# Kernel optimization log

Hardware: AMD Instinct MI355X
Metric: run time of the kernel (lower is better)

The kernel has to match this reference:

```python
import jax, jax.numpy as jnp
import numpy as np

D_MODEL = 256
NUM_UNIVERSES = 8
D_UNIVERSE = D_MODEL // NUM_UNIVERSES
B, S = 1, 1024
TEMP = 5.0
NEG = -1e9


def setup_inputs() -> dict:
    key = jax.random.key(0)
    ks = jax.random.split(key, 5)
    scale = 1.0 / np.sqrt(D_MODEL)
    return {
        "x": jax.random.normal(ks[0], (B, S, D_MODEL), dtype=jnp.float32),
        "Wq": jax.random.normal(ks[1], (D_MODEL, D_MODEL), dtype=jnp.float32) * scale,
        "bq": jnp.zeros((D_MODEL,), dtype=jnp.float32),
        "Wk": jax.random.normal(ks[2], (D_MODEL, D_MODEL), dtype=jnp.float32) * scale,
        "bk": jnp.zeros((D_MODEL,), dtype=jnp.float32),
        "Wv": jax.random.normal(ks[3], (D_MODEL, D_MODEL), dtype=jnp.float32) * scale,
        "bv": jnp.zeros((D_MODEL,), dtype=jnp.float32),
        "Wo": jax.random.normal(ks[4], (D_MODEL, D_MODEL), dtype=jnp.float32) * scale,
        "bo": jnp.zeros((D_MODEL,), dtype=jnp.float32),
    }


def reference(x, Wq, bq, Wk, bk, Wv, bv, Wo, bo):
    b, s, d = x.shape
    h, du = NUM_UNIVERSES, D_UNIVERSE
    # Projections; Q,K squashed to [0,1] fuzzy truth values
    Q = jax.nn.sigmoid(x @ Wq + bq)
    K = jax.nn.sigmoid(x @ Wk + bk)
    V = x @ Wv + bv
    # [B,S,D] -> [B,H,S,du]
    Q = Q.reshape(b, s, h, du).transpose(0, 2, 1, 3)
    K = K.reshape(b, s, h, du).transpose(0, 2, 1, 3)
    V = V.reshape(b, s, h, du).transpose(0, 2, 1, 3)
    # Fuzzy implication: clamp(1 - Q_i + K_j, max=1), mean over d_universe
    # Broadcast to [B,H,S,S,du] (the memory-heavy intermediate)
    implication = jnp.minimum(1.0 - Q[:, :, :, None, :] + K[:, :, None, :, :], 1.0)
    truth = implication.mean(axis=-1)  # [B,H,S,S]
    # Causal mask
    causal = jnp.tril(jnp.ones((s, s), dtype=bool))
    truth = jnp.where(causal[None, None], truth, NEG)
    attn = jax.nn.softmax(truth * TEMP, axis=-1)
    out = jnp.einsum("bhij,bhjd->bhid", attn, V)
    out = out.transpose(0, 2, 1, 3).reshape(b, s, d)
    return out @ Wo + bo
```

## Files before the change

### kernel.cpp

```cpp
#include <hip/hip_runtime.h>
#include <math.h>

#define S_LEN 1024
#define DM    256
#define DU    32
#define TEMPF 5.0f
#define NS    4

__global__ __launch_bounds__(256) void qkv_proj_kernel(
    const float* __restrict__ x,
    const float* __restrict__ Wq, const float* __restrict__ bq,
    const float* __restrict__ Wk, const float* __restrict__ bk,
    const float* __restrict__ Wv, const float* __restrict__ bv,
    float* __restrict__ qo, float* __restrict__ ko, float* __restrict__ vo)
{
    const int mat = blockIdx.z;
    const float* __restrict__ W    = (mat == 0) ? Wq : ((mat == 1) ? Wk : Wv);
    const float* __restrict__ bias = (mat == 0) ? bq : ((mat == 1) ? bk : bv);
    float* __restrict__ dst        = (mat == 0) ? qo : ((mat == 1) ? ko : vo);

    const int n0 = blockIdx.x * 64;
    const int m0 = blockIdx.y * 32;
    const int t  = threadIdx.x;
    const int tx = t & 15;
    const int ty = t >> 4;

    __shared__ float xs[2][32][36];
    __shared__ float wsh[2][32][68];

    float acc[2][4] = {};

    const int xrow = t & 31;
    const int xkc  = (t >> 5) * 4;
    const int wrow = t >> 4;
    const int wcol = (t & 15) * 4;

    float4 xa = *(const float4*)&x[(m0 + xrow) * DM + xkc];
    float4 wa = *(const float4*)&W[wrow * DM + n0 + wcol];
    float4 wb = *(const float4*)&W[(wrow + 16) * DM + n0 + wcol];
    xs[0][xkc + 0][xrow] = xa.x; xs[0][xkc + 1][xrow] = xa.y;
    xs[0][xkc + 2][xrow] = xa.z; xs[0][xkc + 3][xrow] = xa.w;
    *(float4*)&wsh[0][wrow][wcol]      = wa;
    *(float4*)&wsh[0][wrow + 16][wcol] = wb;
    __syncthreads();

    int cur = 0;
    for (int k0 = 32; k0 < DM; k0 += 32) {
        xa = *(const float4*)&x[(m0 + xrow) * DM + k0 + xkc];
        wa = *(const float4*)&W[(k0 + wrow) * DM + n0 + wcol];
        wb = *(const float4*)&W[(k0 + wrow + 16) * DM + n0 + wcol];
        #pragma unroll
        for (int kk = 0; kk < 32; kk++) {
            float2 a2 = *(const float2*)&xs[cur][kk][ty * 2];
            float4 b4 = *(const float4*)&wsh[cur][kk][tx * 4];
            acc[0][0] += a2.x * b4.x; acc[0][1] += a2.x * b4.y;
            acc[0][2] += a2.x * b4.z; acc[0][3] += a2.x * b4.w;
            acc[1][0] += a2.y * b4.x; acc[1][1] += a2.y * b4.y;
            acc[1][2] += a2.y * b4.z; acc[1][3] += a2.y * b4.w;
        }
        const int nxt = cur ^ 1;
        xs[nxt][xkc + 0][xrow] = xa.x; xs[nxt][xkc + 1][xrow] = xa.y;
        xs[nxt][xkc + 2][xrow] = xa.z; xs[nxt][xkc + 3][xrow] = xa.w;
        *(float4*)&wsh[nxt][wrow][wcol]      = wa;
        *(float4*)&wsh[nxt][wrow + 16][wcol] = wb;
        __syncthreads();
        cur = nxt;
    }
    #pragma unroll
    for (int kk = 0; kk < 32; kk++) {
        float2 a2 = *(const float2*)&xs[cur][kk][ty * 2];
        float4 b4 = *(const float4*)&wsh[cur][kk][tx * 4];
        acc[0][0] += a2.x * b4.x; acc[0][1] += a2.x * b4.y;
        acc[0][2] += a2.x * b4.z; acc[0][3] += a2.x * b4.w;
        acc[1][0] += a2.y * b4.x; acc[1][1] += a2.y * b4.y;
        acc[1][2] += a2.y * b4.z; acc[1][3] += a2.y * b4.w;
    }

    #pragma unroll
    for (int j = 0; j < 4; j++) {
        const int cidx = n0 + tx * 4 + j;
        const float bb = bias[cidx];
        const int hh = cidx >> 5;
        const int dd = cidx & 31;
        #pragma unroll
        for (int i = 0; i < 2; i++) {
            const int row = m0 + ty * 2 + i;
            float val = acc[i][j] + bb;
            if (mat < 2) val = 1.0f / (1.0f + __expf(-val));
            dst[hh * (S_LEN * DU) + row * DU + dd] = val;
        }
    }
}

__global__ __launch_bounds__(256) void attn_kernel(
    const float* __restrict__ q, const float* __restrict__ k,
    const float* __restrict__ v,
    float* __restrict__ part_o, float* __restrict__ part_ml)
{
    const int bid = blockIdx.x;
    const int it2 = 31 - (bid >> 5);
    const int sub = bid & 31;
    const int h   = sub & 7;
    const int s   = sub >> 3;
    const int t   = threadIdx.x;
    const int r   = t >> 4;
    const int c   = t & 15;
    const int ig0 = it2 * 32 + r;
    const int ig1 = ig0 + 16;

    __shared__ float  Ks[64][36];
    __shared__ float2 Vs2[64][17];
    __shared__ float  Ps[32][68];

    float qreg0[32], qreg1[32];
    {
        const float* q0 = q + h * (S_LEN * DU) + ig0 * DU;
        const float* q1 = q + h * (S_LEN * DU) + ig1 * DU;
        #pragma unroll
        for (int d4 = 0; d4 < 8; d4++) {
            float4 a = *(const float4*)&q0[d4 * 4];
            float4 b = *(const float4*)&q1[d4 * 4];
            qreg0[d4 * 4 + 0] = a.x; qreg0[d4 * 4 + 1] = a.y;
            qreg0[d4 * 4 + 2] = a.z; qreg0[d4 * 4 + 3] = a.w;
            qreg1[d4 * 4 + 0] = b.x; qreg1[d4 * 4 + 1] = b.y;
            qreg1[d4 * 4 + 2] = b.z; qreg1[d4 * 4 + 3] = b.w;
        }
    }

    float m0r = -1e30f, m1r = -1e30f, l0 = 0.0f, l1 = 0.0f;
    float o00 = 0.0f, o01 = 0.0f, o10 = 0.0f, o11 = 0.0f;

    const int njt = it2 / 2 + 1;
    for (int jt = s; jt < njt; jt += NS) {
        __syncthreads();
        {
            const int jr  = t >> 2;
            const int d0k = (t & 3) * 8;
            const int dv  = (t & 3) * 4;
            const float* kp = k + h * (S_LEN * DU) + (jt * 64 + jr) * DU;
            const float* vp = v + h * (S_LEN * DU) + (jt * 64 + jr) * DU;
            float4 ka = *(const float4*)&kp[d0k];
            float4 kb = *(const float4*)&kp[d0k + 4];
            float4 va4 = *(const float4*)&vp[dv];
            float4 vb4 = *(const float4*)&vp[dv + 16];
            *(float4*)&Ks[jr][d0k]     = ka;
            *(float4*)&Ks[jr][d0k + 4] = kb;
            Vs2[jr][dv + 0] = make_float2(va4.x, vb4.x);
            Vs2[jr][dv + 1] = make_float2(va4.y, vb4.y);
            Vs2[jr][dv + 2] = make_float2(va4.z, vb4.z);
            Vs2[jr][dv + 3] = make_float2(va4.w, vb4.w);
        }
        __syncthreads();

        float zv0[4], zv1[4];
        #pragma unroll
        for (int q4 = 0; q4 < 4; q4++) {
            const int jj  = c + q4 * 16;
            const int jgl = jt * 64 + jj;
            float s0 = 0.0f, s1 = 0.0f;
            #pragma unroll
            for (int d = 0; d < 32; d += 4) {
                float4 k4 = *(const float4*)&Ks[jj][d];
                s0 += fmaxf(qreg0[d + 0] - k4.x, 0.0f)
                    + fmaxf(qreg0[d + 1] - k4.y, 0.0f)
                    + fmaxf(qreg0[d + 2] - k4.z, 0.0f)
                    + fmaxf(qreg0[d + 3] - k4.w, 0.0f);
                s1 += fmaxf(qreg1[d + 0] - k4.x, 0.0f)
                    + fmaxf(qreg1[d + 1] - k4.y, 0.0f)
                    + fmaxf(qreg1[d + 2] - k4.z, 0.0f)
                    + fmaxf(qreg1[d + 3] - k4.w, 0.0f);
            }
            zv0[q4] = (jgl <= ig0) ? (TEMPF - (TEMPF / 32.0f) * s0) : -1e30f;
            zv1[q4] = (jgl <= ig1) ? (TEMPF - (TEMPF / 32.0f) * s1) : -1e30f;
        }

        float mloc0 = fmaxf(fmaxf(zv0[0], zv0[1]), fmaxf(zv0[2], zv0[3]));
        float mloc1 = fmaxf(fmaxf(zv1[0], zv1[1]), fmaxf(zv1[2], zv1[3]));
        #pragma unroll
        for (int off = 8; off; off >>= 1) {
            mloc0 = fmaxf(mloc0, __shfl_xor(mloc0, off, 16));
            mloc1 = fmaxf(mloc1, __shfl_xor(mloc1, off, 16));
        }
        const float mn0 = fmaxf(m0r, mloc0), mn1 = fmaxf(m1r, mloc1);
        const float al0 = __expf(m0r - mn0), al1 = __expf(m1r - mn1);

        float ll0 = 0.0f, ll1 = 0.0f;
        #pragma unroll
        for (int q4 = 0; q4 < 4; q4++) {
            const float p0 = __expf(zv0[q4] - mn0);
            const float p1 = __expf(zv1[q4] - mn1);
            ll0 += p0; ll1 += p1;
            Ps[r][c + q4 * 16]      = p0;
            Ps[r + 16][c + q4 * 16] = p1;
        }
        #pragma unroll
        for (int off = 8; off; off >>= 1) {
            ll0 += __shfl_xor(ll0, off, 16);
            ll1 += __shfl_xor(ll1, off, 16);
        }

        float pv00 = 0.0f, pv01 = 0.0f, pv10 = 0.0f, pv11 = 0.0f;
        #pragma unroll 4
        for (int j4 = 0; j4 < 64; j4 += 4) {
            float4 pj0 = *(const float4*)&Ps[r][j4];
            float4 pj1 = *(const float4*)&Ps[r + 16][j4];
            float2 va = Vs2[j4 + 0][c];
            float2 vb = Vs2[j4 + 1][c];
            float2 vc2 = Vs2[j4 + 2][c];
            float2 vd = Vs2[j4 + 3][c];
            pv00 += pj0.x * va.x + pj0.y * vb.x + pj0.z * vc2.x + pj0.w * vd.x;
            pv01 += pj0.x * va.y + pj0.y * vb.y + pj0.z * vc2.y + pj0.w * vd.y;
            pv10 += pj1.x * va.x + pj1.y * vb.x + pj1.z * vc2.x + pj1.w * vd.x;
            pv11 += pj1.x * va.y + pj1.y * vb.y + pj1.z * vc2.y + pj1.w * vd.y;
        }

        m0r = mn0; l0 = l0 * al0 + ll0; o00 = o00 * al0 + pv00; o01 = o01 * al0 + pv01;
        m1r = mn1; l1 = l1 * al1 + ll1; o10 = o10 * al1 + pv10; o11 = o11 * al1 + pv11;
    }

    const int pbase = (h * 32 + it2) * NS + s;
    float* po = part_o + pbase * 1024;
    po[r * 32 + c]             = o00;
    po[r * 32 + c + 16]        = o01;
    po[(r + 16) * 32 + c]      = o10;
    po[(r + 16) * 32 + c + 16] = o11;
    if (c == 0) {
        *(float2*)&part_ml[pbase * 64 + r * 2]        = make_float2(m0r, l0);
        *(float2*)&part_ml[pbase * 64 + (r + 16) * 2] = make_float2(m1r, l1);
    }
}

__global__ __launch_bounds__(256) void combine_kernel(
    const float* __restrict__ part_o, const float* __restrict__ part_ml,
    float* __restrict__ attn)
{
    const int h   = blockIdx.x & 7;
    const int it2 = blockIdx.x >> 3;
    const int t   = threadIdx.x;
    const int r   = t >> 4;
    const int c   = t & 15;
    const int base = (h * 32 + it2) * NS;

    float2 ml0[NS], ml1[NS];
    #pragma unroll
    for (int s2 = 0; s2 < NS; s2++) {
        ml0[s2] = *(const float2*)&part_ml[(base + s2) * 64 + r * 2];
        ml1[s2] = *(const float2*)&part_ml[(base + s2) * 64 + (r + 16) * 2];
    }
    float M0 = ml0[0].x, M1 = ml1[0].x;
    #pragma unroll
    for (int s2 = 1; s2 < NS; s2++) {
        M0 = fmaxf(M0, ml0[s2].x);
        M1 = fmaxf(M1, ml1[s2].x);
    }
    float L0 = 0.0f, L1 = 0.0f, a00 = 0.0f, a01 = 0.0f, a10 = 0.0f, a11 = 0.0f;
    #pragma unroll
    for (int s2 = 0; s2 < NS; s2++) {
        const float w0 = __expf(ml0[s2].x - M0);
        const float w1 = __expf(ml1[s2].x - M1);
        L0 += w0 * ml0[s2].y;
        L1 += w1 * ml1[s2].y;
        const float* po = part_o + (base + s2) * 1024;
        a00 += w0 * po[r * 32 + c];
        a01 += w0 * po[r * 32 + c + 16];
        a10 += w1 * po[(r + 16) * 32 + c];
        a11 += w1 * po[(r + 16) * 32 + c + 16];
    }
    const float i0 = 1.0f / L0, i1 = 1.0f / L1;
    attn[(it2 * 32 + r) * DM + h * DU + c]           = a00 * i0;
    attn[(it2 * 32 + r) * DM + h * DU + c + 16]      = a01 * i0;
    attn[(it2 * 32 + r + 16) * DM + h * DU + c]      = a10 * i1;
    attn[(it2 * 32 + r + 16) * DM + h * DU + c + 16] = a11 * i1;
}

__global__ __launch_bounds__(256) void out_proj_kernel(
    const float* __restrict__ a, const float* __restrict__ W,
    const float* __restrict__ bias, float* __restrict__ dst)
{
    const int n0 = blockIdx.x * 32;
    const int m0 = blockIdx.y * 32;
    const int t  = threadIdx.x;
    const int tx = t & 15;
    const int ty = t >> 4;

    __shared__ float xs[2][32][36];
    __shared__ float wsh[2][32][36];

    float acc[2][2] = {};

    const int arow = t & 31;
    const int akc  = (t >> 5) * 4;
    const int wr   = t >> 3;
    const int wc   = (t & 7) * 4;

    float4 xa = *(const float4*)&a[(m0 + arow) * DM + akc];
    float4 wa = *(const float4*)&W[wr * DM + n0 + wc];
    xs[0][akc + 0][arow] = xa.x; xs[0][akc + 1][arow] = xa.y;
    xs[0][akc + 2][arow] = xa.z; xs[0][akc + 3][arow] = xa.w;
    *(float4*)&wsh[0][wr][wc] = wa;
    __syncthreads();

    int cur = 0;
    for (int k0 = 32; k0 < DM; k0 += 32) {
        xa = *(const float4*)&a[(m0 + arow) * DM + k0 + akc];
        wa = *(const float4*)&W[(k0 + wr) * DM + n0 + wc];
        #pragma unroll
        for (int kk = 0; kk < 32; kk++) {
            float2 a2 = *(const float2*)&xs[cur][kk][ty * 2];
            float2 b2 = *(const float2*)&wsh[cur][kk][tx * 2];
            acc[0][0] += a2.x * b2.x; acc[0][1] += a2.x * b2.y;
            acc[1][0] += a2.y * b2.x; acc[1][1] += a2.y * b2.y;
        }
        const int nxt = cur ^ 1;
        xs[nxt][akc + 0][arow] = xa.x; xs[nxt][akc + 1][arow] = xa.y;
        xs[nxt][akc + 2][arow] = xa.z; xs[nxt][akc + 3][arow] = xa.w;
        *(float4*)&wsh[nxt][wr][wc] = wa;
        __syncthreads();
        cur = nxt;
    }
    #pragma unroll
    for (int kk = 0; kk < 32; kk++) {
        float2 a2 = *(const float2*)&xs[cur][kk][ty * 2];
        float2 b2 = *(const float2*)&wsh[cur][kk][tx * 2];
        acc[0][0] += a2.x * b2.x; acc[0][1] += a2.x * b2.y;
        acc[1][0] += a2.y * b2.x; acc[1][1] += a2.y * b2.y;
    }

    #pragma unroll
    for (int j = 0; j < 2; j++) {
        const int cidx = n0 + tx * 2 + j;
        const float bb = bias[cidx];
        #pragma unroll
        for (int i = 0; i < 2; i++) {
            const int row = m0 + ty * 2 + i;
            dst[row * DM + cidx] = acc[i][j] + bb;
        }
    }
}

extern "C" void kernel_launch(void* const* d_in, const int* in_sizes, int n_in,
                              void* d_out, int out_size, void* d_ws, size_t ws_size,
                              hipStream_t stream)
{
    const float* x  = (const float*)d_in[0];
    const float* Wq = (const float*)d_in[1];
    const float* bq = (const float*)d_in[2];
    const float* Wk = (const float*)d_in[3];
    const float* bk = (const float*)d_in[4];
    const float* Wv = (const float*)d_in[5];
    const float* bv = (const float*)d_in[6];
    const float* Wo = (const float*)d_in[7];
    const float* bo = (const float*)d_in[8];
    float* out = (float*)d_out;

    float* ws      = (float*)d_ws;
    float* q       = ws;
    float* k       = q + 262144;
    float* v       = k + 262144;
    float* attn    = v + 262144;
    float* part_o  = attn + 262144;
    float* part_ml = part_o + 1048576;

    qkv_proj_kernel<<<dim3(4, 32, 3), 256, 0, stream>>>(x, Wq, bq, Wk, bk, Wv, bv, q, k, v);
    attn_kernel<<<dim3(8 * 32 * NS), 256, 0, stream>>>(q, k, v, part_o, part_ml);
    combine_kernel<<<dim3(256), 256, 0, stream>>>(part_o, part_ml, attn);
    out_proj_kernel<<<dim3(8, 32), 256, 0, stream>>>(attn, Wo, bo, out);
}
```

Before: 119.7 us.

## Enlarge attention query tile, drop online max, prefetch K/V into registers

The attention kernel now processes 64 query rows per block (four per thread) instead of 32, so each K/V tile in shared memory serves twice as many queries. It also drops the running-max rescaling, relying on the fact that scores are bounded by TEMP, and prefetches the next K/V tile into registers while the current one is computed. V is stored in a float4-transposed layout, and the combine kernel reduces to plain sums. The cost is higher register pressure from four 32-float Q arrays under launch_bounds(256,2), plus half as many blocks, which may hurt occupancy and load balance.

Result: no change. 118.6 us (-0.9%).

```diff
diff --git a/kernel.cpp b/kernel.cpp
--- a/kernel.cpp
+++ b/kernel.cpp
@@ -92,185 +92,158 @@
     }
 }
 
-__global__ __launch_bounds__(256) void attn_kernel(
+__global__ __launch_bounds__(256, 2) void attn_kernel(
     const float* __restrict__ q, const float* __restrict__ k,
     const float* __restrict__ v,
-    float* __restrict__ part_o, float* __restrict__ part_ml)
+    float* __restrict__ part_o, float* __restrict__ part_l)
 {
     const int bid = blockIdx.x;
-    const int it2 = 31 - (bid >> 5);
+    const int it4 = 15 - (bid >> 5);
     const int sub = bid & 31;
     const int h   = sub & 7;
     const int s   = sub >> 3;
     const int t   = threadIdx.x;
     const int r   = t >> 4;
     const int c   = t & 15;
-    const int ig0 = it2 * 32 + r;
-    const int ig1 = ig0 + 16;
+    const int i0  = it4 * 64;
 
     __shared__ float  Ks[64][36];
-    __shared__ float2 Vs2[64][17];
-    __shared__ float  Ps[32][68];
-
-    float qreg0[32], qreg1[32];
-    {
-        const float* q0 = q + h * (S_LEN * DU) + ig0 * DU;
-        const float* q1 = q + h * (S_LEN * DU) + ig1 * DU;
+    __shared__ float4 Vs4[16][2][17];
+    __shared__ float  Ps[64][68];
+
+    float qreg[4][32];
+    #pragma unroll
+    for (int kq = 0; kq < 4; kq++) {
+        const float* qrow = q + h * (S_LEN * DU) + (i0 + r + 16 * kq) * DU;
         #pragma unroll
         for (int d4 = 0; d4 < 8; d4++) {
-            float4 a = *(const float4*)&q0[d4 * 4];
-            float4 b = *(const float4*)&q1[d4 * 4];
-            qreg0[d4 * 4 + 0] = a.x; qreg0[d4 * 4 + 1] = a.y;
-            qreg0[d4 * 4 + 2] = a.z; qreg0[d4 * 4 + 3] = a.w;
-            qreg1[d4 * 4 + 0] = b.x; qreg1[d4 * 4 + 1] = b.y;
-            qreg1[d4 * 4 + 2] = b.z; qreg1[d4 * 4 + 3] = b.w;
-        }
-    }
-
-    float m0r = -1e30f, m1r = -1e30f, l0 = 0.0f, l1 = 0.0f;
-    float o00 = 0.0f, o01 = 0.0f, o10 = 0.0f, o11 = 0.0f;
-
-    const int njt = it2 / 2 + 1;
+            float4 qv = *(const float4*)&qrow[d4 * 4];
+            qreg[kq][d4*4+0] = qv.x; qreg[kq][d4*4+1] = qv.y;
+            qreg[kq][d4*4+2] = qv.z; qreg[kq][d4*4+3] = qv.w;
+        }
+    }
+
+    float o0[4] = {0,0,0,0}, o1[4] = {0,0,0,0}, lpart[4] = {0,0,0,0};
+
+    const int jr = t >> 2;
+    const int d0 = (t & 3) * 8;
+    const float* kbase = k + h * (S_LEN * DU);
+    const float* vbase = v + h * (S_LEN * DU);
+
+    const int njt = it4 + 1;
+    float4 ka, kb, va, vb;
+    if (s < njt) {
+        const float* kp = kbase + (s * 64 + jr) * DU + d0;
+        const float* vp = vbase + (s * 64 + jr) * DU + d0;
+        ka = *(const float4*)kp; kb = *(const float4*)(kp + 4);
+        va = *(const float4*)vp; vb = *(const float4*)(vp + 4);
+    }
+
     for (int jt = s; jt < njt; jt += NS) {
         __syncthreads();
+        *(float4*)&Ks[jr][d0]     = ka;
+        *(float4*)&Ks[jr][d0 + 4] = kb;
         {
-            const int jr  = t >> 2;
-            const int d0k = (t & 3) * 8;
-            const int dv  = (t & 3) * 4;
-            const float* kp = k + h * (S_LEN * DU) + (jt * 64 + jr) * DU;
-            const float* vp = v + h * (S_LEN * DU) + (jt * 64 + jr) * DU;
-            float4 ka = *(const float4*)&kp[d0k];
-            float4 kb = *(const float4*)&kp[d0k + 4];
-            float4 va4 = *(const float4*)&vp[dv];
-            float4 vb4 = *(const float4*)&vp[dv + 16];
-            *(float4*)&Ks[jr][d0k]     = ka;
-            *(float4*)&Ks[jr][d0k + 4] = kb;
-            Vs2[jr][dv + 0] = make_float2(va4.x, vb4.x);
-            Vs2[jr][dv + 1] = make_float2(va4.y, vb4.y);
-            Vs2[jr][dv + 2] = make_float2(va4.z, vb4.z);
-            Vs2[jr][dv + 3] = make_float2(va4.w, vb4.w);
+            float vv[8] = {va.x, va.y, va.z, va.w, vb.x, vb.y, vb.z, vb.w};
+            #pragma unroll
+            for (int i = 0; i < 8; i++) {
+                const int d = d0 + i;
+                ((float*)&Vs4[jr >> 2][d >> 4][d & 15])[jr & 3] = vv[i];
+            }
         }
         __syncthreads();
-
-        float zv0[4], zv1[4];
+        if (jt + NS < njt) {
+            const float* kp = kbase + ((jt + NS) * 64 + jr) * DU + d0;
+            const float* vp = vbase + ((jt + NS) * 64 + jr) * DU + d0;
+            ka = *(const float4*)kp; kb = *(const float4*)(kp + 4);
+            va = *(const float4*)vp; vb = *(const float4*)(vp + 4);
+        }
+
         #pragma unroll
         for (int q4 = 0; q4 < 4; q4++) {
             const int jj  = c + q4 * 16;
             const int jgl = jt * 64 + jj;
-            float s0 = 0.0f, s1 = 0.0f;
+            float sacc[4] = {0,0,0,0};
             #pragma unroll
             for (int d = 0; d < 32; d += 4) {
                 float4 k4 = *(const float4*)&Ks[jj][d];
-                s0 += fmaxf(qreg0[d + 0] - k4.x, 0.0f)
-                    + fmaxf(qreg0[d + 1] - k4.y, 0.0f)
-                    + fmaxf(qreg0[d + 2] - k4.z, 0.0f)
-                    + fmaxf(qreg0[d + 3] - k4.w, 0.0f);
-                s1 += fmaxf(qreg1[d + 0] - k4.x, 0.0f)
-                    + fmaxf(qreg1[d + 1] - k4.y, 0.0f)
-                    + fmaxf(qreg1[d + 2] - k4.z, 0.0f)
-                    + fmaxf(qreg1[d + 3] - k4.w, 0.0f);
+                #pragma unroll
+                for (int kq = 0; kq < 4; kq++) {
+                    sacc[kq] += fmaxf(qreg[kq][d+0] - k4.x, 0.0f)
+                              + fmaxf(qreg[kq][d+1] - k4.y, 0.0f)
+                              + fmaxf(qreg[kq][d+2] - k4.z, 0.0f)
+                              + fmaxf(qreg[kq][d+3] - k4.w, 0.0f);
+                }
             }
-            zv0[q4] = (jgl <= ig0) ? (TEMPF - (TEMPF / 32.0f) * s0) : -1e30f;
-            zv1[q4] = (jgl <= ig1) ? (TEMPF - (TEMPF / 32.0f) * s1) : -1e30f;
-        }
-
-        float mloc0 = fmaxf(fmaxf(zv0[0], zv0[1]), fmaxf(zv0[2], zv0[3]));
-        float mloc1 = fmaxf(fmaxf(zv1[0], zv1[1]), fmaxf(zv1[2], zv1[3]));
-        #pragma unroll
-        for (int off = 8; off; off >>= 1) {
-            mloc0 = fmaxf(mloc0, __shfl_xor(mloc0, off, 16));
-            mloc1 = fmaxf(mloc1, __shfl_xor(mloc1, off, 16));
-        }
-        const float mn0 = fmaxf(m0r, mloc0), mn1 = fmaxf(m1r, mloc1);
-        const float al0 = __expf(m0r - mn0), al1 = __expf(m1r - mn1);
-
-        float ll0 = 0.0f, ll1 = 0.0f;
-        #pragma unroll
-        for (int q4 = 0; q4 < 4; q4++) {
-            const float p0 = __expf(zv0[q4] - mn0);
-            const float p1 = __expf(zv1[q4] - mn1);
-            ll0 += p0; ll1 += p1;
-            Ps[r][c + q4 * 16]      = p0;
-            Ps[r + 16][c + q4 * 16] = p1;
-        }
-        #pragma unroll
-        for (int off = 8; off; off >>= 1) {
-            ll0 += __shfl_xor(ll0, off, 16);
-            ll1 += __shfl_xor(ll1, off, 16);
-        }
-
-        float pv00 = 0.0f, pv01 = 0.0f, pv10 = 0.0f, pv11 = 0.0f;
+            #pragma unroll
+            for (int kq = 0; kq < 4; kq++) {
+                const int ig = i0 + r + 16 * kq;
+                const float p = (jgl <= ig)
+                    ? __expf(TEMPF - (TEMPF / 32.0f) * sacc[kq]) : 0.0f;
+                lpart[kq] += p;
+                Ps[r + 16 * kq][jj] = p;
+            }
+        }
+
         #pragma unroll 4
-        for (int j4 = 0; j4 < 64; j4 += 4) {
-            float4 pj0 = *(const float4*)&Ps[r][j4];
-            float4 pj1 = *(const float4*)&Ps[r + 16][j4];
-            float2 va = Vs2[j4 + 0][c];
-            float2 vb = Vs2[j4 + 1][c];
-            float2 vc2 = Vs2[j4 + 2][c];
-            float2 vd = Vs2[j4 + 3][c];
-            pv00 += pj0.x * va.x + pj0.y * vb.x + pj0.z * vc2.x + pj0.w * vd.x;
-            pv01 += pj0.x * va.y + pj0.y * vb.y + pj0.z * vc2.y + pj0.w * vd.y;
-            pv10 += pj1.x * va.x + pj1.y * vb.x + pj1.z * vc2.x + pj1.w * vd.x;
-            pv11 += pj1.x * va.y + pj1.y * vb.y + pj1.z * vc2.y + pj1.w * vd.y;
-        }
-
-        m0r = mn0; l0 = l0 * al0 + ll0; o00 = o00 * al0 + pv00; o01 = o01 * al0 + pv01;
-        m1r = mn1; l1 = l1 * al1 + ll1; o10 = o10 * al1 + pv10; o11 = o11 * al1 + pv11;
-    }
-
-    const int pbase = (h * 32 + it2) * NS + s;
-    float* po = part_o + pbase * 1024;
-    po[r * 32 + c]             = o00;
-    po[r * 32 + c + 16]        = o01;
-    po[(r + 16) * 32 + c]      = o10;
-    po[(r + 16) * 32 + c + 16] = o11;
+        for (int j4 = 0; j4 < 16; j4++) {
+            float4 vA = Vs4[j4][0][c];
+            float4 vB = Vs4[j4][1][c];
+            #pragma unroll
+            for (int kq = 0; kq < 4; kq++) {
+                float4 pj = *(const float4*)&Ps[r + 16 * kq][j4 * 4];
+                o0[kq] += pj.x*vA.x + pj.y*vA.y + pj.z*vA.z + pj.w*vA.w;
+                o1[kq] += pj.x*vB.x + pj.y*vB.y + pj.z*vB.z + pj.w*vB.w;
+            }
+        }
+    }
+
+    #pragma unroll
+    for (int off = 8; off; off >>= 1)
+        #pragma unroll
+        for (int kq = 0; kq < 4; kq++)
+            lpart[kq] += __shfl_xor(lpart[kq], off, 16);
+
+    const int pbase = (h * 16 + it4) * NS + s;
+    float* po = part_o + pbase * 2048;
+    #pragma unroll
+    for (int kq = 0; kq < 4; kq++) {
+        po[(r + 16 * kq) * 32 + c]      = o0[kq];
+        po[(r + 16 * kq) * 32 + c + 16] = o1[kq];
+    }
     if (c == 0) {
-        *(float2*)&part_ml[pbase * 64 + r * 2]        = make_float2(m0r, l0);
-        *(float2*)&part_ml[pbase * 64 + (r + 16) * 2] = make_float2(m1r, l1);
+        #pragma unroll
+        for (int kq = 0; kq < 4; kq++)
+            part_l[pbase * 64 + r + 16 * kq] = lpart[kq];
     }
 }
 
 __global__ __launch_bounds__(256) void combine_kernel(
-    const float* __restrict__ part_o, const float* __restrict__ part_ml,
+    const float* __restrict__ part_o, const float* __restrict__ part_l,
     float* __restrict__ attn)
 {
-    const int h   = blockIdx.x & 7;
-    const int it2 = blockIdx.x >> 3;
-    const int t   = threadIdx.x;
-    const int r   = t >> 4;
-    const int c   = t & 15;
-    const int base = (h * 32 + it2) * NS;
-
-    float2 ml0[NS], ml1[NS];
-    #pragma unroll
-    for (int s2 = 0; s2 < NS; s2++) {
-        ml0[s2] = *(const float2*)&part_ml[(base + s2) * 64 + r * 2];
-        ml1[s2] = *(const float2*)&part_ml[(base + s2) * 64 + (r + 16) * 2];
-    }
-    float M0 = ml0[0].x, M1 = ml1[0].x;
-    #pragma unroll
-    for (int s2 = 1; s2 < NS; s2++) {
-        M0 = fmaxf(M0, ml0[s2].x);
-        M1 = fmaxf(M1, ml1[s2].x);
-    }
-    float L0 = 0.0f, L1 = 0.0f, a00 = 0.0f, a01 = 0.0f, a10 = 0.0f, a11 = 0.0f;
-    #pragma unroll
-    for (int s2 = 0; s2 < NS; s2++) {
-        const float w0 = __expf(ml0[s2].x - M0);
-        const float w1 = __expf(ml1[s2].x - M1);
-        L0 += w0 * ml0[s2].y;
-        L1 += w1 * ml1[s2].y;
-        const float* po = part_o + (base + s2) * 1024;
-        a00 += w0 * po[r * 32 + c];
-        a01 += w0 * po[r * 32 + c + 16];
-        a10 += w1 * po[(r + 16) * 32 + c];
-        a11 += w1 * po[(r + 16) * 32 + c + 16];
-    }
-    const float i0 = 1.0f / L0, i1 = 1.0f / L1;
-    attn[(it2 * 32 + r) * DM + h * DU + c]           = a00 * i0;
-    attn[(it2 * 32 + r) * DM + h * DU + c + 16]      = a01 * i0;
-    attn[(it2 * 32 + r + 16) * DM + h * DU + c]      = a10 * i1;
-    attn[(it2 * 32 + r + 16) * DM + h * DU + c + 16] = a11 * i1;
+    const int h    = blockIdx.x & 7;
+    const int it4  = blockIdx.x >> 3;
+    const int t    = threadIdx.x;
+    const int r    = t >> 4;
+    const int c    = t & 15;
+    const int base = (h * 16 + it4) * NS;
+
+    #pragma unroll
+    for (int kq = 0; kq < 4; kq++) {
+        const int row = r + 16 * kq;
+        float os0 = 0.0f, os1 = 0.0f, ls = 0.0f;
+        #pragma unroll
+        for (int s2 = 0; s2 < NS; s2++) {
+            const float* po = part_o + (base + s2) * 2048;
+            os0 += po[row * 32 + c];
+            os1 += po[row * 32 + c + 16];
+            ls  += part_l[(base + s2) * 64 + row];
+        }
+        const float inv = 1.0f / ls;
+        attn[(it4 * 64 + row) * DM + h * DU + c]      = os0 * inv;
+        attn[(it4 * 64 + row) * DM + h * DU + c + 16] = os1 * inv;
+    }
 }
 
 __global__ __launch_bounds__(256) void out_proj_kernel(
@@ -359,10 +332,10 @@
     float* v       = k + 262144;
     float* attn    = v + 262144;
     float* part_o  = attn + 262144;
-    float* part_ml = part_o + 1048576;
+    float* part_l  = part_o + 1048576;
 
     qkv_proj_kernel<<<dim3(4, 32, 3), 256, 0, stream>>>(x, Wq, bq, Wk, bk, Wv, bv, q, k, v);
-    attn_kernel<<<dim3(8 * 32 * NS), 256, 0, stream>>>(q, k, v, part_o, part_ml);
-    combine_kernel<<<dim3(256), 256, 0, stream>>>(part_o, part_ml, attn);
+    attn_kernel<<<dim3(512), 256, 0, stream>>>(q, k, v, part_o, part_l);
+    combine_kernel<<<dim3(128), 256, 0, stream>>>(part_o, part_l, attn);
     out_proj_kernel<<<dim3(8, 32), 256, 0, stream>>>(attn, Wo, bo, out);
 }
```
